# Kernel tuning notes

Hardware: AMD Instinct MI355X
Metric: run time of the kernel (lower is better)

Reference implementation:

```python
import jax, jax.numpy as jnp
import numpy as np

N = 100000   # nodes
E = 1600000  # edges
D = 128      # feature dim
G = 64       # graphs in batch


def setup_inputs() -> dict:
    key = jax.random.key(0)
    k1, k2, k3, k4, k5, k6, k7, k8 = jax.random.split(key, 8)
    in_feat = jax.random.normal(k1, (N, D), dtype=jnp.float32)
    src = jax.random.randint(k2, (E,), 0, N, dtype=jnp.int32)
    dst = jax.random.randint(k3, (E,), 0, N, dtype=jnp.int32)
    graph_ids = jax.random.randint(k4, (N,), 0, G, dtype=jnp.int32)
    s = 1.0 / np.sqrt(D)
    W1 = jax.random.uniform(k5, (D, D), jnp.float32, -s, s)
    b1 = jnp.zeros((D,), jnp.float32)
    W2 = jax.random.uniform(k6, (D, D), jnp.float32, -s, s)
    b2 = jnp.zeros((D,), jnp.float32)
    return {"in_feat": in_feat, "W1": W1, "b1": b1, "W2": W2, "b2": b2,
            "src": src, "dst": dst, "graph_ids": graph_ids}


def _graph_conv(x, src, dst, W, b, norm_src, norm_dst):
    # DGL GraphConv, norm='both': D_out^{-1/2} A D_in^{-1/2} X W + b
    m = (x * norm_src[:, None])[src]                       # [E, d] gather
    agg = jax.ops.segment_sum(m, dst, num_segments=N)      # [N, d] scatter-add
    return (agg * norm_dst[:, None]) @ W + b


def reference(in_feat, W1, b1, W2, b2, src, dst, graph_ids):
    ones_e = jnp.ones((E,), jnp.float32)
    deg_out = jax.ops.segment_sum(ones_e, src, num_segments=N)
    deg_in = jax.ops.segment_sum(ones_e, dst, num_segments=N)
    norm_src = jnp.where(deg_out > 0, deg_out, 1.0) ** -0.5  # D_out^{-1/2}
    norm_dst = jnp.where(deg_in > 0, deg_in, 1.0) ** -0.5    # D_in^{-1/2}

    h = _graph_conv(in_feat, src, dst, W1, b1, norm_src, norm_dst)
    h = jax.nn.relu(h)
    h = _graph_conv(h, src, dst, W2, b2, norm_src, norm_dst)

    # AvgPooling: per-graph mean over nodes -> [G, D]
    sums = jax.ops.segment_sum(h, graph_ids, num_segments=G)
    counts = jax.ops.segment_sum(jnp.ones((N,), jnp.float32), graph_ids, num_segments=G)
    return sums / jnp.maximum(counts, 1.0)[:, None]
```

## Files before the change

kernel.cpp:

```cpp
#include <hip/hip_runtime.h>
#include <cstdint>


#define DD 128
#define PB 512
#define GB 384
#define KC 32
#define CHK 3200

typedef __attribute__((ext_vector_type(8))) short bf16x8;
typedef __attribute__((ext_vector_type(4))) float f32x4;
typedef __attribute__((ext_vector_type(2))) float f32x2;

__device__ __forceinline__ unsigned short f2bf(float f) {
  union { float f; unsigned u; } v; v.f = f;
  unsigned r = (v.u + 0x7fff + ((v.u >> 16) & 1)) >> 16;
  return (unsigned short)r;
}
__device__ __forceinline__ unsigned cvt_pk_bf16(float lo, float hi) {
  unsigned r;
  asm("v_cvt_pk_bf16_f32 %0, %1, %2" : "=v"(r) : "v"(lo), "v"(hi));
  return r;
}
__device__ __forceinline__ unsigned char f2fp8(float f) {
  return (unsigned char)(__builtin_amdgcn_cvt_pk_fp8_f32(f, f, 0, false) & 0xff);
}

__global__ __launch_bounds__(256) void k_part1a(const int* __restrict__ src, const int* __restrict__ dst,
                                                const int* __restrict__ gid,
                                                unsigned* __restrict__ histD, unsigned* __restrict__ histS,
                                                unsigned* __restrict__ rawD, unsigned* __restrict__ rawS,
                                                int* __restrict__ gcnt, int E, int N, int G) {
  __shared__ unsigned hD[256], hS[256];
  __shared__ int h64[64];
  hD[threadIdx.x] = 0; hS[threadIdx.x] = 0;
  if (threadIdx.x < 64) h64[threadIdx.x] = 0;
  __syncthreads();
  int chunk = (E + gridDim.x - 1) / gridDim.x;
  int e0 = blockIdx.x * chunk, e1 = min(E, e0 + chunk);
  for (int e = e0 + threadIdx.x; e < e1; e += 256) {
    atomicAdd(&hD[(unsigned)dst[e] >> 9], 1u);
    atomicAdd(&hS[(unsigned)src[e] >> 9], 1u);
  }
  int stride = gridDim.x * 256;
  for (int i = blockIdx.x * 256 + threadIdx.x; i < N; i += stride)
    atomicAdd(&h64[gid[i]], 1);
  __syncthreads();
  unsigned vd = hD[threadIdx.x], vs = hS[threadIdx.x];
  histD[blockIdx.x * 256 + threadIdx.x] = vd;
  histS[blockIdx.x * 256 + threadIdx.x] = vs;
  rawD[blockIdx.x * 256 + threadIdx.x] = vd;
  rawS[blockIdx.x * 256 + threadIdx.x] = vs;
  if (threadIdx.x < (unsigned)G) {
    int v = h64[threadIdx.x];
    if (v) atomicAdd(&gcnt[threadIdx.x], v);
  }
}

__global__ __launch_bounds__(256) void k_pscanA(unsigned* __restrict__ histD, unsigned* __restrict__ histS,
                                                unsigned* __restrict__ tot) {
  __shared__ unsigned excl[PB], psc[256];
  int table = blockIdx.x >> 8, b = blockIdx.x & 255;
  unsigned* hist = table ? histS : histD;
  int t = threadIdx.x;
  unsigned s0 = hist[(2 * t) * 256 + b];
  unsigned s1 = hist[(2 * t + 1) * 256 + b];
  unsigned pr = s0 + s1;
  psc[t] = pr;
  __syncthreads();
  for (int off = 1; off < 256; off <<= 1) {
    unsigned x = (t >= off) ? psc[t - off] : 0;
    __syncthreads();
    psc[t] += x;
    __syncthreads();
  }
  unsigned pex = psc[t] - pr;
  excl[2 * t] = pex;
  excl[2 * t + 1] = pex + s0;
  __syncthreads();
  hist[(2 * t) * 256 + b] = excl[2 * t];
  hist[(2 * t + 1) * 256 + b] = excl[2 * t + 1];
  if (t == 255) tot[table * 256 + b] = psc[255];
}

__global__ __launch_bounds__(256) void k_pscanB(const unsigned* __restrict__ tot,
                                                int* __restrict__ bsD, int* __restrict__ bsS) {
  __shared__ unsigned s[256];
  int t = threadIdx.x;
#pragma unroll
  for (int table = 0; table < 2; ++table) {
    int* bs = table ? bsS : bsD;
    unsigned v = tot[table * 256 + t];
    s[t] = v;
    __syncthreads();
    for (int off = 1; off < 256; off <<= 1) {
      unsigned x = (t >= off) ? s[t - off] : 0;
      __syncthreads();
      s[t] += x;
      __syncthreads();
    }
    bs[t] = (int)(s[t] - v);
    if (t == 255) bs[256] = (int)s[255];
    __syncthreads();
  }
}

__global__ __launch_bounds__(256) void k_part1c(const int* __restrict__ src, const int* __restrict__ dst,
                                                const unsigned* __restrict__ histD, const unsigned* __restrict__ histS,
                                                const unsigned* __restrict__ rawD, const unsigned* __restrict__ rawS,
                                                const int* __restrict__ bsD, const int* __restrict__ bsS,
                                                unsigned* __restrict__ pairD, unsigned* __restrict__ pairS, int E) {
  __shared__ unsigned pkD[CHK], pkS[CHK];
  __shared__ unsigned char bkD[CHK], bkS[CHK];
  __shared__ unsigned curD[256], curS[256], gbD[256], gbS[256], psc[256];
  int chunk = (E + gridDim.x - 1) / gridDim.x;
  int e0 = blockIdx.x * chunk, e1 = min(E, e0 + chunk);
  int n = e1 - e0;
  int t = threadIdx.x;
  unsigned vD = rawD[blockIdx.x * 256 + t];
  psc[t] = vD;
  __syncthreads();
  for (int off = 1; off < 256; off <<= 1) {
    unsigned x = (t >= off) ? psc[t - off] : 0;
    __syncthreads();
    psc[t] += x;
    __syncthreads();
  }
  unsigned exD = psc[t] - vD;
  curD[t] = exD;
  gbD[t] = histD[blockIdx.x * 256 + t] + (unsigned)bsD[t] - exD;
  __syncthreads();
  unsigned vS = rawS[blockIdx.x * 256 + t];
  psc[t] = vS;
  __syncthreads();
  for (int off = 1; off < 256; off <<= 1) {
    unsigned x = (t >= off) ? psc[t - off] : 0;
    __syncthreads();
    psc[t] += x;
    __syncthreads();
  }
  unsigned exS = psc[t] - vS;
  curS[t] = exS;
  gbS[t] = histS[blockIdx.x * 256 + t] + (unsigned)bsS[t] - exS;
  __syncthreads();
  for (int i = t; i < n; i += 256) {
    unsigned sv = (unsigned)src[e0 + i], dv = (unsigned)dst[e0 + i];
    unsigned bD = dv >> 9, bS = sv >> 9;
    unsigned pD = atomicAdd(&curD[bD], 1u);
    pkD[pD] = ((dv & 511u) << 17) | sv;
    bkD[pD] = (unsigned char)bD;
    unsigned pS = atomicAdd(&curS[bS], 1u);
    pkS[pS] = ((sv & 511u) << 17) | dv;
    bkS[pS] = (unsigned char)bS;
  }
  __syncthreads();
  for (int i = t; i < n; i += 256)
    pairD[gbD[bkD[i]] + i] = pkD[i];
  for (int i = t; i < n; i += 256)
    pairS[gbS[bkS[i]] + i] = pkS[i];
}

__global__ __launch_bounds__(256) void k_part2d(const unsigned* __restrict__ pairD, const int* __restrict__ bsD,
                                                const int* __restrict__ gcnt, const int* __restrict__ gid,
                                                int* __restrict__ offs, float* __restrict__ ndst,
                                                uint2* __restrict__ pwg, int* __restrict__ degI,
                                                int* __restrict__ dbin,
                                                int* __restrict__ srcS, int N) {
  __shared__ unsigned hist[512], excl[512], psc[256];
  __shared__ int ldb[256];
  int k = blockIdx.x, base = k << 9;
  int b0 = bsD[k], b1 = bsD[k + 1];
  hist[threadIdx.x] = 0; hist[threadIdx.x + 256] = 0;
  ldb[threadIdx.x] = 0;
  __syncthreads();
  for (int i = b0 + threadIdx.x; i < b1; i += 256)
    atomicAdd(&hist[pairD[i] >> 17], 1u);
  __syncthreads();
  unsigned s0 = hist[2 * threadIdx.x], s1 = hist[2 * threadIdx.x + 1];
  unsigned pr = s0 + s1;
  psc[threadIdx.x] = pr;
  __syncthreads();
  for (int off = 1; off < 256; off <<= 1) {
    unsigned x = (threadIdx.x >= off) ? psc[threadIdx.x - off] : 0;
    __syncthreads();
    psc[threadIdx.x] += x;
    __syncthreads();
  }
  unsigned pex = psc[threadIdx.x] - pr;
  excl[2 * threadIdx.x] = pex;
  excl[2 * threadIdx.x + 1] = pex + s0;
  __syncthreads();
  for (int j = threadIdx.x; j < 512; j += 256) {
    int node = base + j;
    if (node <= N) offs[node] = b0 + (int)excl[j];
    if (node < N) {
      int dg = (int)hist[j];
      degI[node] = dg;
      atomicAdd(&ldb[255 - min(dg, 255)], 1);
      float gi = (float)dg; gi = gi > 0.f ? gi : 1.f;
      float nd = rsqrtf(gi);
      ndst[node] = nd;
      float c = (float)gcnt[gid[node]]; c = c > 1.f ? c : 1.f;
      float w = nd / c;
      union { float f; unsigned u; } v; v.f = w;
      pwg[node] = make_uint2(v.u, (unsigned)gid[node]);
    }
  }
  __syncthreads();
  if (ldb[threadIdx.x]) atomicAdd(&dbin[threadIdx.x], ldb[threadIdx.x]);
  for (int i = b0 + threadIdx.x; i < b1; i += 256) {
    unsigned pkv = pairD[i];
    unsigned pos = atomicAdd(&excl[pkv >> 17], 1u);
    srcS[b0 + (int)pos] = (int)(pkv & 0x1FFFFu);
  }
}

__global__ __launch_bounds__(256) void k_dscan(const int* __restrict__ dbin, int* __restrict__ dcur) {
  __shared__ int s[256];
  int t = threadIdx.x;
  int v = dbin[t];
  s[t] = v;
  __syncthreads();
  for (int off = 1; off < 256; off <<= 1) {
    int x = (t >= off) ? s[t - off] : 0;
    __syncthreads();
    s[t] += x;
    __syncthreads();
  }
  dcur[t] = s[t] - v;
}

__global__ __launch_bounds__(256) void k_dperm(const int* __restrict__ degI, int* __restrict__ dcur,
                                               int* __restrict__ perm, int N) {
  __shared__ int lh[256], lcur[256];
  int t = threadIdx.x, i = blockIdx.x * 256 + t;
  lh[t] = 0;
  __syncthreads();
  int bin = 0;
  if (i < N) {
    bin = 255 - min(degI[i], 255);
    atomicAdd(&lh[bin], 1);
  }
  __syncthreads();
  int r = lh[t] ? atomicAdd(&dcur[t], lh[t]) : 0;
  lcur[t] = r;
  __syncthreads();
  if (i < N) {
    int pos = atomicAdd(&lcur[bin], 1);
    perm[pos] = i;
  }
}

__global__ __launch_bounds__(1024, 1) void k_pw(const unsigned* __restrict__ pairS, const int* __restrict__ bsS,
                                                const uint2* __restrict__ pwg,
                                                unsigned short* __restrict__ P16,
                                                float* __restrict__ nsrc, int N) {
  __shared__ float tile[512 * 64];
  __shared__ unsigned hist[512];
  int k = blockIdx.x, base = k << 9;
  int b0 = bsS[k], b1 = bsS[k + 1];
  for (int i = threadIdx.x; i < 512 * 64; i += 1024) tile[i] = 0.f;
  if (threadIdx.x < 512) hist[threadIdx.x] = 0;
  __syncthreads();
  for (int i = b0 + threadIdx.x; i < b1; i += 1024) {
    unsigned pkv = pairS[i];
    unsigned dv = pkv & 0x1FFFFu;
    unsigned sloc = pkv >> 17;
    atomicAdd(&hist[sloc], 1u);
    uint2 u = pwg[dv];
    union { unsigned u; float f; } w; w.u = u.x;
    atomicAdd(&tile[sloc * 64 + u.y], w.f);
  }
  __syncthreads();
  if (threadIdx.x < 512) {
    int node = base + threadIdx.x;
    if (node < N) {
      float g = (float)hist[threadIdx.x]; g = g > 0.f ? g : 1.f;
      nsrc[node] = rsqrtf(g);
    }
  }
  for (int grp = threadIdx.x; grp < 4096; grp += 1024) {
    int qb = grp >> 6, g = grp & 63;
    unsigned w0 = cvt_pk_bf16(tile[(qb * 8 + 0) * 64 + g], tile[(qb * 8 + 1) * 64 + g]);
    unsigned w1 = cvt_pk_bf16(tile[(qb * 8 + 2) * 64 + g], tile[(qb * 8 + 3) * 64 + g]);
    unsigned w2 = cvt_pk_bf16(tile[(qb * 8 + 4) * 64 + g], tile[(qb * 8 + 5) * 64 + g]);
    unsigned w3 = cvt_pk_bf16(tile[(qb * 8 + 6) * 64 + g], tile[(qb * 8 + 7) * 64 + g]);
    uint4 o = make_uint4(w0, w1, w2, w3);
    *(uint4*)(P16 + ((size_t)(base >> 3) + qb) * 512 + g * 8) = o;
  }
}

__global__ __launch_bounds__(128) void k_wprep(const float* __restrict__ W, unsigned short* __restrict__ Wt,
                                               unsigned char* __restrict__ zrow) {
  int n = blockIdx.x, k = threadIdx.x;
  Wt[n * 128 + k] = f2bf(W[k * 128 + n]);
  if (n == 0) zrow[k] = 0;
}

__global__ __launch_bounds__(256) void k_gemm1(const float* __restrict__ X, const unsigned short* __restrict__ Wt,
                                               const float* __restrict__ nsrc,
                                               unsigned char* __restrict__ Z8, int N) {
  __shared__ unsigned short Wl[128 * 128];
  int wave = threadIdx.x >> 6, lane = threadIdx.x & 63;
  int quad = lane >> 4, l16 = lane & 15;
  int row0 = blockIdx.x * 64 + wave * 16;
  int arow = row0 + l16; if (arow >= N) arow = N - 1;
  const float* xr = X + (size_t)arow * 128 + quad * 8;
  float4 xv[8];
#pragma unroll
  for (int kbi = 0; kbi < 4; ++kbi) {
    xv[2 * kbi]     = *(const float4*)(xr + kbi * 32);
    xv[2 * kbi + 1] = *(const float4*)(xr + kbi * 32 + 4);
  }
  for (int i = threadIdx.x; i < 2048; i += 256) {
    int wrow = i >> 4, sgrp = i & 15;
    *(uint4*)(Wl + wrow * 128 + ((sgrp ^ (wrow & 15)) << 3)) = ((const uint4*)Wt)[i];
  }
  __syncthreads();
  f32x4 acc[8];
#pragma unroll
  for (int i = 0; i < 8; ++i) acc[i] = (f32x4){0.f, 0.f, 0.f, 0.f};
#pragma unroll
  for (int kbi = 0; kbi < 4; ++kbi) {
    float4 x0 = xv[2 * kbi], x1 = xv[2 * kbi + 1];
    union { unsigned u[4]; bf16x8 v; } A;
    A.u[0] = cvt_pk_bf16(x0.x, x0.y);
    A.u[1] = cvt_pk_bf16(x0.z, x0.w);
    A.u[2] = cvt_pk_bf16(x1.x, x1.y);
    A.u[3] = cvt_pk_bf16(x1.z, x1.w);
#pragma unroll
    for (int nt = 0; nt < 8; ++nt) {
      bf16x8 b = *(const bf16x8*)(Wl + (nt * 16 + l16) * 128 + (((kbi * 4 + quad) ^ l16) << 3));
      acc[nt] = __builtin_amdgcn_mfma_f32_16x16x32_bf16(A.v, b, acc[nt], 0, 0, 0);
    }
  }
  int rbase = row0 + quad * 4;
#pragma unroll
  for (int r = 0; r < 4; ++r) {
    int row = rbase + r;
    if (row < N) {
      float s = nsrc[row];
#pragma unroll
      for (int nt = 0; nt < 8; ++nt)
        Z8[(size_t)row * 128 + nt * 16 + l16] = f2fp8(acc[nt][r] * s);
    }
  }
}

#define ACC16(u) do {                                             \
    c0 += __builtin_amdgcn_cvt_pk_f32_fp8((u).x, false);          \
    c1 += __builtin_amdgcn_cvt_pk_f32_fp8((u).x, true);           \
    c2 += __builtin_amdgcn_cvt_pk_f32_fp8((u).y, false);          \
    c3 += __builtin_amdgcn_cvt_pk_f32_fp8((u).y, true);           \
    c4 += __builtin_amdgcn_cvt_pk_f32_fp8((u).z, false);          \
    c5 += __builtin_amdgcn_cvt_pk_f32_fp8((u).z, true);           \
    c6 += __builtin_amdgcn_cvt_pk_f32_fp8((u).w, false);          \
    c7 += __builtin_amdgcn_cvt_pk_f32_fp8((u).w, true);           \
  } while (0)

__global__ __launch_bounds__(256) void k_layer1(const unsigned char* __restrict__ Z8,
                                                const int* __restrict__ offs, const int* __restrict__ srcS,
                                                const int* __restrict__ perm,
                                                const float* __restrict__ b1,
                                                const float* __restrict__ nsrc, const float* __restrict__ ndst,
                                                unsigned short* __restrict__ Hb, int N) {
  int lane = threadIdx.x & 63;
  int oct = lane >> 3, l8 = lane & 7;
  int dd = blockIdx.x * 32 + (threadIdx.x >> 6) * 8 + oct;
  bool live = dd < N;
  int pd = perm[live ? dd : 0];
  int start = offs[pd];
  int end = live ? offs[pd + 1] : start;
  const int f = l8 * 16;
  const unsigned char* zb = Z8 + f;
  float nd = ndst[pd], ns = nsrc[pd];
  f32x2 c0 = {0.f, 0.f}, c1 = {0.f, 0.f}, c2 = {0.f, 0.f}, c3 = {0.f, 0.f};
  f32x2 c4 = {0.f, 0.f}, c5 = {0.f, 0.f}, c6 = {0.f, 0.f}, c7 = {0.f, 0.f};
  int e = start;
  int rem = end - start;
  int s0 = N, s1 = N, s2 = N, s3 = N;
  if (rem > 0) s0 = srcS[e];
  if (rem > 1) s1 = srcS[e + 1];
  if (rem > 2) s2 = srcS[e + 2];
  if (rem > 3) s3 = srcS[e + 3];
  while (__any(rem > 0)) {
    uint4 u0 = *(const uint4*)(zb + ((size_t)s0 << 7));
    uint4 u1 = *(const uint4*)(zb + ((size_t)s1 << 7));
    uint4 u2 = *(const uint4*)(zb + ((size_t)s2 << 7));
    uint4 u3 = *(const uint4*)(zb + ((size_t)s3 << 7));
    int n0 = N, n1 = N, n2 = N, n3 = N;
    if (rem > 4) n0 = srcS[e + 4];
    if (rem > 5) n1 = srcS[e + 5];
    if (rem > 6) n2 = srcS[e + 6];
    if (rem > 7) n3 = srcS[e + 7];
    ACC16(u0);
    ACC16(u1);
    ACC16(u2);
    ACC16(u3);
    s0 = n0; s1 = n1; s2 = n2; s3 = n3;
    e += 4;
    rem -= 4;
  }
  if (live) {
    float4 bv0 = *(const float4*)(b1 + f);
    float4 bv1 = *(const float4*)(b1 + f + 4);
    float4 bv2 = *(const float4*)(b1 + f + 8);
    float4 bv3 = *(const float4*)(b1 + f + 12);
    float h0 = fmaxf(fmaf(nd, c0[0], bv0.x), 0.f) * ns;
    float h1 = fmaxf(fmaf(nd, c0[1], bv0.y), 0.f) * ns;
    float h2 = fmaxf(fmaf(nd, c1[0], bv0.z), 0.f) * ns;
    float h3 = fmaxf(fmaf(nd, c1[1], bv0.w), 0.f) * ns;
    float h4 = fmaxf(fmaf(nd, c2[0], bv1.x), 0.f) * ns;
    float h5 = fmaxf(fmaf(nd, c2[1], bv1.y), 0.f) * ns;
    float h6 = fmaxf(fmaf(nd, c3[0], bv1.z), 0.f) * ns;
    float h7 = fmaxf(fmaf(nd, c3[1], bv1.w), 0.f) * ns;
    float h8 = fmaxf(fmaf(nd, c4[0], bv2.x), 0.f) * ns;
    float h9 = fmaxf(fmaf(nd, c4[1], bv2.y), 0.f) * ns;
    float hA = fmaxf(fmaf(nd, c5[0], bv2.z), 0.f) * ns;
    float hB = fmaxf(fmaf(nd, c5[1], bv2.w), 0.f) * ns;
    float hC = fmaxf(fmaf(nd, c6[0], bv3.x), 0.f) * ns;
    float hD = fmaxf(fmaf(nd, c6[1], bv3.y), 0.f) * ns;
    float hE = fmaxf(fmaf(nd, c7[0], bv3.z), 0.f) * ns;
    float hF = fmaxf(fmaf(nd, c7[1], bv3.w), 0.f) * ns;
    unsigned short* hrow = Hb + (size_t)pd * 128 + f;
    *(uint4*)hrow = make_uint4(cvt_pk_bf16(h0, h1), cvt_pk_bf16(h2, h3),
                               cvt_pk_bf16(h4, h5), cvt_pk_bf16(h6, h7));
    *(uint4*)(hrow + 8) = make_uint4(cvt_pk_bf16(h8, h9), cvt_pk_bf16(hA, hB),
                                     cvt_pk_bf16(hC, hD), cvt_pk_bf16(hE, hF));
  }
}

__global__ __launch_bounds__(256) void k_poolgemm(const unsigned short* __restrict__ P16,
                                                  const unsigned short* __restrict__ Hb,
                                                  float* __restrict__ pooled, int N, int Kpad, int chunk) {
  __shared__ unsigned short Hl[KC * 128];
  int t = threadIdx.x;
  int r0 = blockIdx.x * chunk;
  int r1 = min(Kpad, r0 + chunk);
  int wv = t >> 6, lane = t & 63, quad = lane >> 4, l16 = lane & 15;
  f32x4 acc[8];
#pragma unroll
  for (int i = 0; i < 8; ++i) acc[i] = (f32x4){0.f, 0.f, 0.f, 0.f};
  for (int rb = r0; rb < r1; rb += KC) {
    int r = t >> 3, c = (t & 7) * 16;
    int cs = c ^ ((r >> 3) * 16);
    int row = rb + r;
    if (row < N) {
      const uint4* srcp = (const uint4*)(Hb + (size_t)row * 128 + c);
      *(uint4*)(Hl + r * 128 + cs) = srcp[0];
      *(uint4*)(Hl + r * 128 + cs + 8) = srcp[1];
    } else {
      uint4 z = make_uint4(0, 0, 0, 0);
      *(uint4*)(Hl + r * 128 + cs) = z;
      *(uint4*)(Hl + r * 128 + cs + 8) = z;
    }
    __syncthreads();
    bf16x8 a = *(const bf16x8*)(P16 + ((size_t)(rb >> 3) + quad) * 512 + (wv * 16 + l16) * 8);
#pragma unroll
    for (int ft = 0; ft < 8; ++ft) {
      bf16x8 b;
#pragma unroll
      for (int j = 0; j < 8; ++j) {
        int rr = quad * 8 + j;
        b[j] = (short)Hl[rr * 128 + ((ft ^ (rr >> 3)) * 16) + l16];
      }
      acc[ft] = __builtin_amdgcn_mfma_f32_16x16x32_bf16(a, b, acc[ft], 0, 0, 0);
    }
    __syncthreads();
  }
#pragma unroll
  for (int ft = 0; ft < 8; ++ft)
#pragma unroll
    for (int rg = 0; rg < 4; ++rg)
      unsafeAtomicAdd(&pooled[(wv * 16 + quad * 4 + rg) * DD + ft * 16 + l16], acc[ft][rg]);
}

__global__ __launch_bounds__(128) void k_out(const float* __restrict__ pooled, const float* __restrict__ W2,
                                             const float* __restrict__ b2, float* __restrict__ out) {
  __shared__ float p[DD];
  int g = blockIdx.x, d = threadIdx.x;
  p[d] = pooled[g * DD + d];
  __syncthreads();
  float a = b2[d];
#pragma unroll 4
  for (int k = 0; k < DD; ++k) a = fmaf(p[k], W2[k * DD + d], a);
  out[g * DD + d] = a;
}

extern "C" void kernel_launch(void* const* d_in, const int* in_sizes, int n_in,
                              void* d_out, int out_size, void* d_ws, size_t ws_size,
                              hipStream_t stream) {
  const float* X  = (const float*)d_in[0];
  const float* W1 = (const float*)d_in[1];
  const float* b1 = (const float*)d_in[2];
  const float* W2 = (const float*)d_in[3];
  const float* b2 = (const float*)d_in[4];
  const int* src  = (const int*)d_in[5];
  const int* dst  = (const int*)d_in[6];
  const int* gid  = (const int*)d_in[7];
  int E = in_sizes[5];
  int N = in_sizes[7];
  int G = out_size / DD;
  int nb = (N >> 9) + 1;
  int Kpad = nb << 9;
  int chunk = ((Kpad + GB * KC - 1) / (GB * KC)) * KC;

  char* w = (char*)d_ws;
  size_t o = 0;
  auto carve = [&](size_t bytes) { char* p = w + o; o += (bytes + 255) & ~(size_t)255; return p; };
  int*   gcnt   = (int*)  carve((size_t)G * 4);
  float* pooled = (float*)carve((size_t)G * DD * 4);
  int*   dbin   = (int*)  carve(256 * 4);
  size_t zeroBytes = o;
  unsigned* histD = (unsigned*)carve((size_t)PB * 256 * 4);
  unsigned* histS = (unsigned*)carve((size_t)PB * 256 * 4);
  unsigned* rawD  = (unsigned*)carve((size_t)PB * 256 * 4);
  unsigned* rawS  = (unsigned*)carve((size_t)PB * 256 * 4);
  unsigned* tot   = (unsigned*)carve(512 * 4);
  int*   bsD    = (int*)  carve(257 * 4);
  int*   bsS    = (int*)  carve(257 * 4);
  int*   dcur   = (int*)  carve(256 * 4);
  unsigned* pairD = (unsigned*)carve((size_t)E * 4);
  unsigned* pairS = (unsigned*)carve((size_t)E * 4);
  int*   srcS   = (int*)  carve((size_t)E * 4);
  int*   offs   = (int*)  carve((size_t)(N + 1) * 4);
  int*   degI   = (int*)  carve((size_t)N * 4);
  int*   perm   = (int*)  carve((size_t)N * 4);
  float* nsrc   = (float*)carve((size_t)N * 4);
  float* ndst   = (float*)carve((size_t)N * 4);
  uint2* pwg    = (uint2*)carve((size_t)N * 8);
  unsigned short* Wt = (unsigned short*)carve(128 * 128 * 2);
  unsigned char*  Z8 = (unsigned char*)carve((size_t)(N + 1) * DD);
  unsigned short* Hb = (unsigned short*)carve((size_t)N * DD * 2);
  unsigned short* P16 = (unsigned short*)carve((size_t)Kpad * 64 * 2);

  hipMemsetAsync(d_ws, 0, zeroBytes, stream);

  k_part1a<<<PB, 256, 0, stream>>>(src, dst, gid, histD, histS, rawD, rawS, gcnt, E, N, G);
  k_pscanA<<<512, 256, 0, stream>>>(histD, histS, tot);
  k_pscanB<<<1, 256, 0, stream>>>(tot, bsD, bsS);
  k_part1c<<<PB, 256, 0, stream>>>(src, dst, histD, histS, rawD, rawS, bsD, bsS, pairD, pairS, E);
  k_part2d<<<nb, 256, 0, stream>>>(pairD, bsD, gcnt, gid, offs, ndst, pwg, degI, dbin, srcS, N);
  k_dscan<<<1, 256, 0, stream>>>(dbin, dcur);
  k_dperm<<<(N + 255) / 256, 256, 0, stream>>>(degI, dcur, perm, N);
  k_pw<<<nb, 1024, 0, stream>>>(pairS, bsS, pwg, P16, nsrc, N);
  k_wprep<<<128, 128, 0, stream>>>(W1, Wt, Z8 + (size_t)N * DD);
  k_gemm1<<<(N + 63) / 64, 256, 0, stream>>>(X, Wt, nsrc, Z8, N);
  k_layer1<<<(N + 31) / 32, 256, 0, stream>>>(Z8, offs, srcS, perm, b1, nsrc, ndst, Hb, N);
  k_poolgemm<<<GB, 256, 0, stream>>>(P16, Hb, pooled, N, Kpad, chunk);
  k_out<<<G, DD, 0, stream>>>(pooled, W2, b2, (float*)d_out);
}
```

Before: 276.2 us.

## Fold weight prep into histogram kernel, enlarge gemm1 blocks, grid-stride layer1

```diff
diff --git a/kernel.cpp b/kernel.cpp
--- a/kernel.cpp
+++ b/kernel.cpp
@@ -30,19 +30,29 @@
                                                 const int* __restrict__ gid,
                                                 unsigned* __restrict__ histD, unsigned* __restrict__ histS,
                                                 unsigned* __restrict__ rawD, unsigned* __restrict__ rawS,
-                                                int* __restrict__ gcnt, int E, int N, int G) {
+                                                int* __restrict__ gcnt,
+                                                const float* __restrict__ W1, unsigned short* __restrict__ Wt,
+                                                unsigned char* __restrict__ zrow,
+                                                int E, int N, int G) {
+  if (blockIdx.x >= PB) {
+    int wb = blockIdx.x - PB;
+    int n = wb * 2 + (threadIdx.x >> 7), k = threadIdx.x & 127;
+    Wt[n * 128 + k] = f2bf(W1[k * 128 + n]);
+    if (wb == 0 && threadIdx.x < 128) zrow[threadIdx.x] = 0;
+    return;
+  }
   __shared__ unsigned hD[256], hS[256];
   __shared__ int h64[64];
   hD[threadIdx.x] = 0; hS[threadIdx.x] = 0;
   if (threadIdx.x < 64) h64[threadIdx.x] = 0;
   __syncthreads();
-  int chunk = (E + gridDim.x - 1) / gridDim.x;
+  int chunk = (E + PB - 1) / PB;
   int e0 = blockIdx.x * chunk, e1 = min(E, e0 + chunk);
   for (int e = e0 + threadIdx.x; e < e1; e += 256) {
     atomicAdd(&hD[(unsigned)dst[e] >> 9], 1u);
     atomicAdd(&hS[(unsigned)src[e] >> 9], 1u);
   }
-  int stride = gridDim.x * 256;
+  int stride = PB * 256;
   for (int i = blockIdx.x * 256 + threadIdx.x; i < N; i += stride)
     atomicAdd(&h64[gid[i]], 1);
   __syncthreads();
@@ -290,20 +300,13 @@
   }
 }
 
-__global__ __launch_bounds__(128) void k_wprep(const float* __restrict__ W, unsigned short* __restrict__ Wt,
-                                               unsigned char* __restrict__ zrow) {
-  int n = blockIdx.x, k = threadIdx.x;
-  Wt[n * 128 + k] = f2bf(W[k * 128 + n]);
-  if (n == 0) zrow[k] = 0;
-}
-
-__global__ __launch_bounds__(256) void k_gemm1(const float* __restrict__ X, const unsigned short* __restrict__ Wt,
+__global__ __launch_bounds__(512) void k_gemm1(const float* __restrict__ X, const unsigned short* __restrict__ Wt,
                                                const float* __restrict__ nsrc,
                                                unsigned char* __restrict__ Z8, int N) {
   __shared__ unsigned short Wl[128 * 128];
   int wave = threadIdx.x >> 6, lane = threadIdx.x & 63;
   int quad = lane >> 4, l16 = lane & 15;
-  int row0 = blockIdx.x * 64 + wave * 16;
+  int row0 = blockIdx.x * 128 + wave * 16;
   int arow = row0 + l16; if (arow >= N) arow = N - 1;
   const float* xr = X + (size_t)arow * 128 + quad * 8;
   float4 xv[8];
@@ -312,7 +315,14 @@
     xv[2 * kbi]     = *(const float4*)(xr + kbi * 32);
     xv[2 * kbi + 1] = *(const float4*)(xr + kbi * 32 + 4);
   }
-  for (int i = threadIdx.x; i < 2048; i += 256) {
+  int rbase = row0 + quad * 4;
+  float sc[4];
+#pragma unroll
+  for (int r = 0; r < 4; ++r) {
+    int row = rbase + r; if (row >= N) row = N - 1;
+    sc[r] = nsrc[row];
+  }
+  for (int i = threadIdx.x; i < 2048; i += 512) {
     int wrow = i >> 4, sgrp = i & 15;
     *(uint4*)(Wl + wrow * 128 + ((sgrp ^ (wrow & 15)) << 3)) = ((const uint4*)Wt)[i];
   }
@@ -334,12 +344,11 @@
       acc[nt] = __builtin_amdgcn_mfma_f32_16x16x32_bf16(A.v, b, acc[nt], 0, 0, 0);
     }
   }
-  int rbase = row0 + quad * 4;
 #pragma unroll
   for (int r = 0; r < 4; ++r) {
     int row = rbase + r;
     if (row < N) {
-      float s = nsrc[row];
+      float s = sc[r];
 #pragma unroll
       for (int nt = 0; nt < 8; ++nt)
         Z8[(size_t)row * 128 + nt * 16 + l16] = f2fp8(acc[nt][r] * s);
@@ -366,67 +375,70 @@
                                                 unsigned short* __restrict__ Hb, int N) {
   int lane = threadIdx.x & 63;
   int oct = lane >> 3, l8 = lane & 7;
-  int dd = blockIdx.x * 32 + (threadIdx.x >> 6) * 8 + oct;
-  bool live = dd < N;
-  int pd = perm[live ? dd : 0];
-  int start = offs[pd];
-  int end = live ? offs[pd + 1] : start;
   const int f = l8 * 16;
   const unsigned char* zb = Z8 + f;
-  float nd = ndst[pd], ns = nsrc[pd];
-  f32x2 c0 = {0.f, 0.f}, c1 = {0.f, 0.f}, c2 = {0.f, 0.f}, c3 = {0.f, 0.f};
-  f32x2 c4 = {0.f, 0.f}, c5 = {0.f, 0.f}, c6 = {0.f, 0.f}, c7 = {0.f, 0.f};
-  int e = start;
-  int rem = end - start;
-  int s0 = N, s1 = N, s2 = N, s3 = N;
-  if (rem > 0) s0 = srcS[e];
-  if (rem > 1) s1 = srcS[e + 1];
-  if (rem > 2) s2 = srcS[e + 2];
-  if (rem > 3) s3 = srcS[e + 3];
-  while (__any(rem > 0)) {
-    uint4 u0 = *(const uint4*)(zb + ((size_t)s0 << 7));
-    uint4 u1 = *(const uint4*)(zb + ((size_t)s1 << 7));
-    uint4 u2 = *(const uint4*)(zb + ((size_t)s2 << 7));
-    uint4 u3 = *(const uint4*)(zb + ((size_t)s3 << 7));
-    int n0 = N, n1 = N, n2 = N, n3 = N;
-    if (rem > 4) n0 = srcS[e + 4];
-    if (rem > 5) n1 = srcS[e + 5];
-    if (rem > 6) n2 = srcS[e + 6];
-    if (rem > 7) n3 = srcS[e + 7];
-    ACC16(u0);
-    ACC16(u1);
-    ACC16(u2);
-    ACC16(u3);
-    s0 = n0; s1 = n1; s2 = n2; s3 = n3;
-    e += 4;
-    rem -= 4;
-  }
-  if (live) {
-    float4 bv0 = *(const float4*)(b1 + f);
-    float4 bv1 = *(const float4*)(b1 + f + 4);
-    float4 bv2 = *(const float4*)(b1 + f + 8);
-    float4 bv3 = *(const float4*)(b1 + f + 12);
-    float h0 = fmaxf(fmaf(nd, c0[0], bv0.x), 0.f) * ns;
-    float h1 = fmaxf(fmaf(nd, c0[1], bv0.y), 0.f) * ns;
-    float h2 = fmaxf(fmaf(nd, c1[0], bv0.z), 0.f) * ns;
-    float h3 = fmaxf(fmaf(nd, c1[1], bv0.w), 0.f) * ns;
-    float h4 = fmaxf(fmaf(nd, c2[0], bv1.x), 0.f) * ns;
-    float h5 = fmaxf(fmaf(nd, c2[1], bv1.y), 0.f) * ns;
-    float h6 = fmaxf(fmaf(nd, c3[0], bv1.z), 0.f) * ns;
-    float h7 = fmaxf(fmaf(nd, c3[1], bv1.w), 0.f) * ns;
-    float h8 = fmaxf(fmaf(nd, c4[0], bv2.x), 0.f) * ns;
-    float h9 = fmaxf(fmaf(nd, c4[1], bv2.y), 0.f) * ns;
-    float hA = fmaxf(fmaf(nd, c5[0], bv2.z), 0.f) * ns;
-    float hB = fmaxf(fmaf(nd, c5[1], bv2.w), 0.f) * ns;
-    float hC = fmaxf(fmaf(nd, c6[0], bv3.x), 0.f) * ns;
-    float hD = fmaxf(fmaf(nd, c6[1], bv3.y), 0.f) * ns;
-    float hE = fmaxf(fmaf(nd, c7[0], bv3.z), 0.f) * ns;
-    float hF = fmaxf(fmaf(nd, c7[1], bv3.w), 0.f) * ns;
-    unsigned short* hrow = Hb + (size_t)pd * 128 + f;
-    *(uint4*)hrow = make_uint4(cvt_pk_bf16(h0, h1), cvt_pk_bf16(h2, h3),
-                               cvt_pk_bf16(h4, h5), cvt_pk_bf16(h6, h7));
-    *(uint4*)(hrow + 8) = make_uint4(cvt_pk_bf16(h8, h9), cvt_pk_bf16(hA, hB),
-                                     cvt_pk_bf16(hC, hD), cvt_pk_bf16(hE, hF));
+  int gstride = gridDim.x * 32;
+  for (int base = blockIdx.x * 32; base < N; base += gstride) {
+    int dd = base + (threadIdx.x >> 6) * 8 + oct;
+    bool live = dd < N;
+    int pd = perm[live ? dd : 0];
+    int start = offs[pd];
+    int end = live ? offs[pd + 1] : start;
+    float nd = ndst[pd], ns = nsrc[pd];
+    f32x2 c0 = {0.f, 0.f}, c1 = {0.f, 0.f}, c2 = {0.f, 0.f}, c3 = {0.f, 0.f};
+    f32x2 c4 = {0.f, 0.f}, c5 = {0.f, 0.f}, c6 = {0.f, 0.f}, c7 = {0.f, 0.f};
+    int e = start;
+    int rem = end - start;
+    int s0 = N, s1 = N, s2 = N, s3 = N;
+    if (rem > 0) s0 = srcS[e];
+    if (rem > 1) s1 = srcS[e + 1];
+    if (rem > 2) s2 = srcS[e + 2];
+    if (rem > 3) s3 = srcS[e + 3];
+    while (__any(rem > 0)) {
+      uint4 u0 = *(const uint4*)(zb + ((size_t)s0 << 7));
+      uint4 u1 = *(const uint4*)(zb + ((size_t)s1 << 7));
+      uint4 u2 = *(const uint4*)(zb + ((size_t)s2 << 7));
+      uint4 u3 = *(const uint4*)(zb + ((size_t)s3 << 7));
+      int n0 = N, n1 = N, n2 = N, n3 = N;
+      if (rem > 4) n0 = srcS[e + 4];
+      if (rem > 5) n1 = srcS[e + 5];
+      if (rem > 6) n2 = srcS[e + 6];
+      if (rem > 7) n3 = srcS[e + 7];
+      ACC16(u0);
+      ACC16(u1);
+      ACC16(u2);
+      ACC16(u3);
+      s0 = n0; s1 = n1; s2 = n2; s3 = n3;
+      e += 4;
+      rem -= 4;
+    }
+    if (live) {
+      float4 bv0 = *(const float4*)(b1 + f);
+      float4 bv1 = *(const float4*)(b1 + f + 4);
+      float4 bv2 = *(const float4*)(b1 + f + 8);
+      float4 bv3 = *(const float4*)(b1 + f + 12);
+      float h0 = fmaxf(fmaf(nd, c0[0], bv0.x), 0.f) * ns;
+      float h1 = fmaxf(fmaf(nd, c0[1], bv0.y), 0.f) * ns;
+      float h2 = fmaxf(fmaf(nd, c1[0], bv0.z), 0.f) * ns;
+      float h3 = fmaxf(fmaf(nd, c1[1], bv0.w), 0.f) * ns;
+      float h4 = fmaxf(fmaf(nd, c2[0], bv1.x), 0.f) * ns;
+      float h5 = fmaxf(fmaf(nd, c2[1], bv1.y), 0.f) * ns;
+      float h6 = fmaxf(fmaf(nd, c3[0], bv1.z), 0.f) * ns;
+      float h7 = fmaxf(fmaf(nd, c3[1], bv1.w), 0.f) * ns;
+      float h8 = fmaxf(fmaf(nd, c4[0], bv2.x), 0.f) * ns;
+      float h9 = fmaxf(fmaf(nd, c4[1], bv2.y), 0.f) * ns;
+      float hA = fmaxf(fmaf(nd, c5[0], bv2.z), 0.f) * ns;
+      float hB = fmaxf(fmaf(nd, c5[1], bv2.w), 0.f) * ns;
+      float hC = fmaxf(fmaf(nd, c6[0], bv3.x), 0.f) * ns;
+      float hD = fmaxf(fmaf(nd, c6[1], bv3.y), 0.f) * ns;
+      float hE = fmaxf(fmaf(nd, c7[0], bv3.z), 0.f) * ns;
+      float hF = fmaxf(fmaf(nd, c7[1], bv3.w), 0.f) * ns;
+      unsigned short* hrow = Hb + (size_t)pd * 128 + f;
+      *(uint4*)hrow = make_uint4(cvt_pk_bf16(h0, h1), cvt_pk_bf16(h2, h3),
+                                 cvt_pk_bf16(h4, h5), cvt_pk_bf16(h6, h7));
+      *(uint4*)(hrow + 8) = make_uint4(cvt_pk_bf16(h8, h9), cvt_pk_bf16(hA, hB),
+                                       cvt_pk_bf16(hC, hD), cvt_pk_bf16(hE, hF));
+    }
   }
 }
 
@@ -536,7 +548,8 @@
 
   hipMemsetAsync(d_ws, 0, zeroBytes, stream);
 
-  k_part1a<<<PB, 256, 0, stream>>>(src, dst, gid, histD, histS, rawD, rawS, gcnt, E, N, G);
+  k_part1a<<<PB + 64, 256, 0, stream>>>(src, dst, gid, histD, histS, rawD, rawS, gcnt,
+                                        W1, Wt, Z8 + (size_t)N * DD, E, N, G);
   k_pscanA<<<512, 256, 0, stream>>>(histD, histS, tot);
   k_pscanB<<<1, 256, 0, stream>>>(tot, bsD, bsS);
   k_part1c<<<PB, 256, 0, stream>>>(src, dst, histD, histS, rawD, rawS, bsD, bsS, pairD, pairS, E);
@@ -544,9 +557,8 @@
   k_dscan<<<1, 256, 0, stream>>>(dbin, dcur);
   k_dperm<<<(N + 255) / 256, 256, 0, stream>>>(degI, dcur, perm, N);
   k_pw<<<nb, 1024, 0, stream>>>(pairS, bsS, pwg, P16, nsrc, N);
-  k_wprep<<<128, 128, 0, stream>>>(W1, Wt, Z8 + (size_t)N * DD);
-  k_gemm1<<<(N + 63) / 64, 256, 0, stream>>>(X, Wt, nsrc, Z8, N);
-  k_layer1<<<(N + 31) / 32, 256, 0, stream>>>(Z8, offs, srcS, perm, b1, nsrc, ndst, Hb, N);
+  k_gemm1<<<(N + 127) / 128, 512, 0, stream>>>(X, Wt, nsrc, Z8, N);
+  k_layer1<<<1024, 256, 0, stream>>>(Z8, offs, srcS, perm, b1, nsrc, ndst, Hb, N);
   k_poolgemm<<<GB, 256, 0, stream>>>(P16, Hb, pooled, N, Kpad, chunk);
   k_out<<<G, DD, 0, stream>>>(pooled, W2, b2, (float*)d_out);
 }
```

New measurement: 272.3 us. About the same (-1.4%).
